# Kernel tuning notes

Hardware: AMD Instinct MI355X
Metric: run time of the kernel (lower is better)

The kernel has to match this reference:

```python
import jax, jax.numpy as jnp
import numpy as np

D_MODEL = 1024
NUM_HEADS = 16


def setup_inputs() -> dict:
    key = jax.random.key(0)
    k1, k2, k3, k4, k5 = jax.random.split(key, 5)
    b, n, d = 4, 2048, D_MODEL
    s = 1.0 / np.sqrt(d)
    x = jax.random.normal(k1, (b, n, d), dtype=jnp.float32)
    v_w = jax.random.uniform(k2, (d, d), dtype=jnp.float32, minval=-s, maxval=s)  # Linear weight [out,in]
    v_b = jax.random.uniform(k3, (d,), dtype=jnp.float32, minval=-s, maxval=s)
    o_w = jax.random.uniform(k4, (d, d), dtype=jnp.float32, minval=-s, maxval=s)
    o_b = jax.random.uniform(k5, (d,), dtype=jnp.float32, minval=-s, maxval=s)
    return {"x": x, "v_w": v_w, "v_b": v_b, "o_w": o_w, "o_b": o_b}


def reference(x, v_w, v_b, o_w, o_b):
    b, n, d = x.shape
    h = NUM_HEADS
    dh = d // h
    # shared QKV projection: q = k = v
    v = jnp.einsum('bnd,ed->bne', x, v_w) + v_b            # [b,n,d]
    v = v.reshape(b, n, h, dh).transpose(0, 2, 1, 3)        # [b,h,n,dh]
    scale = 1.0 / jnp.sqrt(jnp.asarray(dh, dtype=x.dtype))
    scores = jnp.einsum('bhnd,bhmd->bhnm', v, v) * scale    # [b,h,n,n]
    attn = jax.nn.softmax(scores, axis=-1)
    out = jnp.einsum('bhnm,bhmd->bhnd', attn, v)            # [b,h,n,dh]
    out = out.transpose(0, 2, 1, 3).reshape(b, n, d)        # concat heads
    return jnp.einsum('bnd,ed->bne', out, o_w) + o_b
```

## Files before the change

kernel.cpp:

```cpp
#include <hip/hip_runtime.h>
#include <stdint.h>

typedef __attribute__((ext_vector_type(8))) short short8;
typedef __attribute__((ext_vector_type(4))) float f32x4;
typedef __attribute__((ext_vector_type(4))) unsigned int u32x4;
typedef __attribute__((ext_vector_type(2))) unsigned int u32x2;

#define MFMA16(a, b, c) __builtin_amdgcn_mfma_f32_16x16x32_bf16((a), (b), (c), 0, 0, 0)

#define GLD_LDS16(g, l)                                                                  \
    __builtin_amdgcn_global_load_lds((const __attribute__((address_space(1))) void*)(g), \
                                     (__attribute__((address_space(3))) void*)(l), 16, 0, 0)

#if defined(__has_builtin)
#if __has_builtin(__builtin_amdgcn_exp2f)
#define FAST_EXP2(x) __builtin_amdgcn_exp2f(x)
#endif
#endif
#ifndef FAST_EXP2
__device__ __forceinline__ float fast_exp2_asm(float x) {
    float r;
    asm volatile("v_exp_f32 %0, %1\ns_nop 1" : "=v"(r) : "v"(x));
    return r;
}
#define FAST_EXP2(x) fast_exp2_asm(x)
#endif

__device__ __forceinline__ float bf2f(unsigned short u) {
    unsigned int x = ((unsigned int)u) << 16;
    float f;
    __builtin_memcpy(&f, &x, 4);
    return f;
}
__device__ __forceinline__ unsigned short f2bf(float f) {
    unsigned int x;
    __builtin_memcpy(&x, &f, 4);
    unsigned int r = x + 0x7FFFu + ((x >> 16) & 1u);
    return (unsigned short)(r >> 16);
}
__device__ __forceinline__ unsigned int pack2bf(float a, float b) {
    unsigned int ua, ub;
    __builtin_memcpy(&ua, &a, 4);
    __builtin_memcpy(&ub, &b, 4);
    return __builtin_amdgcn_perm(ub + 0x8000u, ua + 0x8000u, 0x07060302u);
}
__device__ __forceinline__ unsigned int cvtpk_bf16(float a, float b) {
    unsigned int r;
    asm("v_cvt_pk_bf16_f32 %0, %1, %2" : "=v"(r) : "v"(a), "v"(b));
    return r;
}
__device__ __forceinline__ u32x4 cvt8(const float* p) {
    f32x4 g0 = *(const f32x4*)p;
    f32x4 g1 = *(const f32x4*)(p + 4);
    u32x4 r;
    r.x = pack2bf(g0[0], g0[1]);
    r.y = pack2bf(g0[2], g0[3]);
    r.z = pack2bf(g1[0], g1[1]);
    r.w = pack2bf(g1[2], g1[3]);
    return r;
}

__global__ __launch_bounds__(256) void cvt_kernel(const float* __restrict__ in,
                                                  unsigned short* __restrict__ out, int n8) {
    int i = blockIdx.x * 256 + threadIdx.x;
    if (i < n8) *(u32x4*)(out + (size_t)i * 8) = cvt8(in + (size_t)i * 8);
}

template <int MODE>
__global__ __launch_bounds__(256) void gemm_dma_kernel(
    const unsigned short* __restrict__ A, const unsigned short* __restrict__ B,
    const float* __restrict__ bias, void* __restrict__ Cv, int M, int N, int K) {
    __shared__ __align__(16) unsigned short As[2][2][128 * 32];
    __shared__ __align__(16) unsigned short Bs[2][2][128 * 32];

    const int tid = threadIdx.x;
    const int wave = tid >> 6, lane = tid & 63;
    const int l15 = lane & 15, quad = lane >> 4;
    const int m0 = blockIdx.x * 128, n0 = blockIdx.y * 128;
    const int wm = (wave >> 1) * 64, wn = (wave & 1) * 64;

    const int row0 = tid >> 2, c0 = (tid & 3) * 8;
    const unsigned short* Ag0 = A + (size_t)(m0 + row0) * K + c0;
    const unsigned short* Ag1 = A + (size_t)(m0 + row0 + 64) * K + c0;
    const unsigned short* Bg0 = B + (size_t)(n0 + row0) * K + c0;
    const unsigned short* Bg1 = B + (size_t)(n0 + row0 + 64) * K + c0;
    const int wl = wave * 512;

#define STAGE(s, k0)                                     \
    do {                                                 \
        GLD_LDS16(Ag0 + (k0), &As[s][0][wl]);            \
        GLD_LDS16(Ag1 + (k0), &As[s][0][2048 + wl]);     \
        GLD_LDS16(Ag0 + (k0) + 32, &As[s][1][wl]);       \
        GLD_LDS16(Ag1 + (k0) + 32, &As[s][1][2048 + wl]); \
        GLD_LDS16(Bg0 + (k0), &Bs[s][0][wl]);            \
        GLD_LDS16(Bg1 + (k0), &Bs[s][0][2048 + wl]);     \
        GLD_LDS16(Bg0 + (k0) + 32, &Bs[s][1][wl]);       \
        GLD_LDS16(Bg1 + (k0) + 32, &Bs[s][1][2048 + wl]); \
    } while (0)

    f32x4 acc[4][4];
#pragma unroll
    for (int i = 0; i < 4; i++)
#pragma unroll
        for (int j = 0; j < 4; j++) {
            f32x4 z = {0.f, 0.f, 0.f, 0.f};
            acc[i][j] = z;
        }

    STAGE(0, 0);
    for (int k0 = 0; k0 < K; k0 += 64) {
        const int s = (k0 >> 6) & 1;
        __syncthreads();
        if (k0 + 64 < K) STAGE(s ^ 1, k0 + 64);

        short8 a0[4], a1[4], b0[4], b1[4];
#pragma unroll
        for (int mt = 0; mt < 4; mt++) {
            a0[mt] = *(const short8*)&As[s][0][(wm + mt * 16 + l15) * 32 + quad * 8];
            a1[mt] = *(const short8*)&As[s][1][(wm + mt * 16 + l15) * 32 + quad * 8];
        }
#pragma unroll
        for (int nt = 0; nt < 4; nt++) {
            b0[nt] = *(const short8*)&Bs[s][0][(wn + nt * 16 + l15) * 32 + quad * 8];
            b1[nt] = *(const short8*)&Bs[s][1][(wn + nt * 16 + l15) * 32 + quad * 8];
        }
#pragma unroll
        for (int mt = 0; mt < 4; mt++)
#pragma unroll
            for (int nt = 0; nt < 4; nt++) acc[mt][nt] = MFMA16(a0[mt], b0[nt], acc[mt][nt]);
#pragma unroll
        for (int mt = 0; mt < 4; mt++)
#pragma unroll
            for (int nt = 0; nt < 4; nt++) acc[mt][nt] = MFMA16(a1[mt], b1[nt], acc[mt][nt]);
    }
#undef STAGE

    float bv[4];
#pragma unroll
    for (int nt = 0; nt < 4; nt++) bv[nt] = bias[n0 + wn + nt * 16 + l15];

#pragma unroll
    for (int mt = 0; mt < 4; mt++)
#pragma unroll
        for (int nt = 0; nt < 4; nt++)
#pragma unroll
            for (int i = 0; i < 4; i++) {
                int m = m0 + wm + mt * 16 + quad * 4 + i;
                int n = n0 + wn + nt * 16 + l15;
                float val = acc[mt][nt][i] + bv[nt];
                if (MODE == 0) {
                    int bb = m >> 11, ns = m & 2047, h = n >> 6, c = n & 63;
                    ((unsigned short*)Cv)[(size_t)(bb * 16 + h) * 131072 + (size_t)ns * 64 + c] =
                        f2bf(val);
                } else {
                    ((float*)Cv)[(size_t)m * N + n] = val;
                }
            }
}

template <bool AF32, bool BF32, int MODE>
__global__ __launch_bounds__(256) void gemm_bias_kernel(
    const void* __restrict__ Av, const void* __restrict__ Bv,
    const float* __restrict__ bias, void* __restrict__ Cv, int M, int N, int K) {
    __shared__ __align__(16) unsigned short As[128][40];
    __shared__ __align__(16) unsigned short Bs[128][40];

    const int tid = threadIdx.x;
    const int wave = tid >> 6, lane = tid & 63;
    const int l15 = lane & 15, quad = lane >> 4;
    const int m0 = blockIdx.x * 128, n0 = blockIdx.y * 128;
    const int wm = (wave >> 1) * 64, wn = (wave & 1) * 64;

    f32x4 acc[4][4];
#pragma unroll
    for (int i = 0; i < 4; i++)
#pragma unroll
        for (int j = 0; j < 4; j++) {
            f32x4 z = {0.f, 0.f, 0.f, 0.f};
            acc[i][j] = z;
        }

    for (int k0 = 0; k0 < K; k0 += 32) {
        __syncthreads();
#pragma unroll
        for (int rep = 0; rep < 2; rep++) {
            int chunk = tid + rep * 256;
            int row = chunk >> 2, c8 = (chunk & 3) * 8;
            if (AF32) {
                const float* Af = (const float*)Av;
                *(u32x4*)&As[row][c8] = cvt8(&Af[(size_t)(m0 + row) * K + k0 + c8]);
            } else {
                const unsigned short* Ab = (const unsigned short*)Av;
                *(f32x4*)&As[row][c8] = *(const f32x4*)&Ab[(size_t)(m0 + row) * K + k0 + c8];
            }
            if (BF32) {
                const float* Bf = (const float*)Bv;
                *(u32x4*)&Bs[row][c8] = cvt8(&Bf[(size_t)(n0 + row) * K + k0 + c8]);
            } else {
                const unsigned short* Bb = (const unsigned short*)Bv;
                *(f32x4*)&Bs[row][c8] = *(const f32x4*)&Bb[(size_t)(n0 + row) * K + k0 + c8];
            }
        }
        __syncthreads();

        short8 a[4], b[4];
#pragma unroll
        for (int mt = 0; mt < 4; mt++) a[mt] = *(const short8*)&As[wm + mt * 16 + l15][quad * 8];
#pragma unroll
        for (int nt = 0; nt < 4; nt++) b[nt] = *(const short8*)&Bs[wn + nt * 16 + l15][quad * 8];
#pragma unroll
        for (int mt = 0; mt < 4; mt++)
#pragma unroll
            for (int nt = 0; nt < 4; nt++) acc[mt][nt] = MFMA16(a[mt], b[nt], acc[mt][nt]);
    }

    float bv[4];
#pragma unroll
    for (int nt = 0; nt < 4; nt++) bv[nt] = bias[n0 + wn + nt * 16 + l15];

#pragma unroll
    for (int mt = 0; mt < 4; mt++)
#pragma unroll
        for (int nt = 0; nt < 4; nt++)
#pragma unroll
            for (int i = 0; i < 4; i++) {
                int m = m0 + wm + mt * 16 + quad * 4 + i;
                int n = n0 + wn + nt * 16 + l15;
                float val = acc[mt][nt][i] + bv[nt];
                if (MODE == 0) {
                    int bb = m >> 11, ns = m & 2047, h = n >> 6, c = n & 63;
                    ((unsigned short*)Cv)[(size_t)(bb * 16 + h) * 131072 + (size_t)ns * 64 + c] =
                        f2bf(val);
                } else {
                    ((float*)Cv)[(size_t)m * N + n] = val;
                }
            }
}

__global__ __launch_bounds__(256) void transpose_kernel(const unsigned short* __restrict__ V,
                                                        unsigned short* __restrict__ Vt) {
    __shared__ __align__(16) unsigned short T[64][72];
    const int tid = threadIdx.x;
    const int n0 = blockIdx.x * 64;
    const size_t base = (size_t)blockIdx.y * 131072;
#pragma unroll
    for (int rep = 0; rep < 2; rep++) {
        int chunk = tid + rep * 256;
        int row = chunk >> 3, c8 = (chunk & 7) * 8;
        *(short8*)&T[row][c8] = *(const short8*)&V[base + (size_t)(n0 + row) * 64 + c8];
    }
    __syncthreads();
#pragma unroll
    for (int rep = 0; rep < 2; rep++) {
        int chunk = tid + rep * 256;
        int d = chunk >> 3, n8 = (chunk & 7) * 8;
        short8 o;
#pragma unroll
        for (int j = 0; j < 8; j++) o[j] = (short)T[n8 + j][d];
        *(short8*)&Vt[base + (size_t)d * 2048 + n0 + n8] = o;
    }
}

__global__ __launch_bounds__(256, 4) void attn_kernel(const unsigned short* __restrict__ V,
                                                      const unsigned short* __restrict__ Vt,
                                                      unsigned short* __restrict__ O) {
    __shared__ __align__(16) unsigned short QP[128 * 64];
    __shared__ __align__(16) unsigned short Ks[64 * 64];
    __shared__ __align__(16) unsigned short VTs[2][64 * 64];

    const int tid = threadIdx.x;
    const int wave = tid >> 6, lane = tid & 63;
    const int l15 = lane & 15, quad = lane >> 4;
    const int sx = l15 & 7;

    const int flat = blockIdx.y * 16 + blockIdx.x;
    const int bh = (flat & 7) * 8 + ((flat >> 3) & 7);
    const int q0 = (flat >> 6) * 128;

    const unsigned short* Vh = V + (size_t)bh * 131072;
    const unsigned short* VhT = Vt + (size_t)bh * 131072;
    const int wm = wave * 32;

    const int srow = wave * 16 + (lane >> 3);
    const int scol = ((lane & 7) ^ (lane >> 3)) * 8;
    const unsigned short* gK = Vh + (size_t)srow * 64 + scol;
    const unsigned short* gVT = VhT + (size_t)srow * 2048 + scol;

#define KSTAGE(kv)                                                       \
    do {                                                                 \
        GLD_LDS16(gK + (size_t)(kv) * 64, &Ks[wave * 1024]);             \
        GLD_LDS16(gK + (size_t)(kv) * 64 + 512, &Ks[wave * 1024 + 512]); \
    } while (0)
#define VSTAGE(s, kv)                                                 \
    do {                                                              \
        GLD_LDS16(gVT + (kv), &VTs[s][wave * 1024]);                  \
        GLD_LDS16(gVT + (kv) + 8 * 2048, &VTs[s][wave * 1024 + 512]); \
    } while (0)

    KSTAGE(0);
    VSTAGE(0, 0);

#pragma unroll
    for (int rep = 0; rep < 4; rep++) {
        int chunk = tid + rep * 256;
        int row = chunk >> 3, cs = chunk & 7;
        short8 g = *(const short8*)&Vh[(size_t)(q0 + row) * 64 + cs * 8];
        short8 o;
#pragma unroll
        for (int j = 0; j < 8; j++)
            o[j] = (short)f2bf(bf2f((unsigned short)g[j]) * 0.1803368801f);
        *(short8*)&QP[row * 64 + ((cs ^ (row & 7)) << 3)] = o;
    }
    __syncthreads();

    short8 bq[2][2];
#pragma unroll
    for (int mt = 0; mt < 2; mt++) {
        const int row = wm + mt * 16 + l15;
#pragma unroll
        for (int ks = 0; ks < 2; ks++)
            bq[mt][ks] = *(const short8*)&QP[row * 64 + ((((ks << 2) | quad) ^ sx) << 3)];
    }

    short8 vones;
#pragma unroll
    for (int j = 0; j < 8; j++) vones[j] = (short)0x3F80;

    f32x4 oacc[2][4];
    f32x4 lsacc[2];
#pragma unroll
    for (int mt = 0; mt < 2; mt++) {
        f32x4 z = {0.f, 0.f, 0.f, 0.f};
        lsacc[mt] = z;
#pragma unroll
        for (int ct = 0; ct < 4; ct++) oacc[mt][ct] = z;
    }

    for (int kv0 = 0; kv0 < 2048; kv0 += 64) {
        const int s = (kv0 >> 6) & 1;
        __syncthreads();
        if (kv0 + 64 < 2048) VSTAGE(s ^ 1, kv0 + 64);

        f32x4 st[4][2];
#pragma unroll
        for (int nt = 0; nt < 4; nt++) {
            const int krow = (nt * 16 + l15) * 64;
            short8 ak0 = *(const short8*)&Ks[krow + ((quad ^ sx) << 3)];
            short8 ak1 = *(const short8*)&Ks[krow + (((4 | quad) ^ sx) << 3)];
#pragma unroll
            for (int mt = 0; mt < 2; mt++) {
                f32x4 z = {0.f, 0.f, 0.f, 0.f};
                z = MFMA16(ak0, bq[mt][0], z);
                z = MFMA16(ak1, bq[mt][1], z);
                st[nt][mt] = z;
            }
        }

        __builtin_amdgcn_sched_barrier(0);
        __builtin_amdgcn_s_barrier();
        __builtin_amdgcn_sched_barrier(0);
        if (kv0 + 64 < 2048) KSTAGE(kv0 + 64);

#pragma unroll
        for (int mt = 0; mt < 2; mt++) {
            const int prow = (wm + mt * 16 + l15) * 64;
#pragma unroll
            for (int nt = 0; nt < 4; nt++) {
                f32x4 p;
#pragma unroll
                for (int i = 0; i < 4; i++) p[i] = FAST_EXP2(st[nt][mt][i]);
                u32x2 w;
                w.x = cvtpk_bf16(p[0], p[1]);
                w.y = cvtpk_bf16(p[2], p[3]);
                const int slot = (nt * 2 + (quad >> 1)) ^ sx;
                *(u32x2*)&QP[prow + slot * 8 + (quad & 1) * 4] = w;
            }
        }
        asm volatile("s_waitcnt lgkmcnt(0)" ::: "memory");

#pragma unroll
        for (int kt = 0; kt < 2; kt++) {
            short8 ap[2];
#pragma unroll
            for (int mt = 0; mt < 2; mt++) {
                const int row = wm + mt * 16 + l15;
                ap[mt] = *(const short8*)&QP[row * 64 + ((((kt << 2) | quad) ^ sx) << 3)];
            }
#pragma unroll
            for (int ct = 0; ct < 4; ct++) {
                short8 bvf =
                    *(const short8*)&VTs[s][(ct * 16 + l15) * 64 + ((((kt << 2) | quad) ^ sx) << 3)];
#pragma unroll
                for (int mt = 0; mt < 2; mt++) oacc[mt][ct] = MFMA16(ap[mt], bvf, oacc[mt][ct]);
            }
#pragma unroll
            for (int mt = 0; mt < 2; mt++) lsacc[mt] = MFMA16(ap[mt], vones, lsacc[mt]);
        }
    }
#undef KSTAGE
#undef VSTAGE

    float inv[2][4];
#pragma unroll
    for (int mt = 0; mt < 2; mt++)
#pragma unroll
        for (int i = 0; i < 4; i++) inv[mt][i] = 1.0f / lsacc[mt][i];

    const int bb = bh >> 4, h = bh & 15;
#pragma unroll
    for (int mt = 0; mt < 2; mt++)
#pragma unroll
        for (int i = 0; i < 4; i++) {
            int m = q0 + wm + mt * 16 + quad * 4 + i;
            size_t rowbase = ((size_t)(bb * 2048 + m)) * 1024 + h * 64;
#pragma unroll
            for (int ct = 0; ct < 4; ct++)
                O[rowbase + ct * 16 + l15] = f2bf(oacc[mt][ct][i] * inv[mt][i]);
        }
}

extern "C" void kernel_launch(void* const* d_in, const int* in_sizes, int n_in, void* d_out,
                              int out_size, void* d_ws, size_t ws_size, hipStream_t stream) {
    (void)in_sizes; (void)n_in; (void)out_size;
    const float* x = (const float*)d_in[0];
    const float* v_w = (const float*)d_in[1];
    const float* v_b = (const float*)d_in[2];
    const float* o_w = (const float*)d_in[3];
    const float* o_b = (const float*)d_in[4];
    float* out = (float*)d_out;

    unsigned short* Vbuf = (unsigned short*)d_out;
    unsigned short* Vtbuf = Vbuf + (size_t)8192 * 1024;
    unsigned short* Obuf = (unsigned short*)d_ws;

    const size_t need =
        ((size_t)8192 * 1024  + (size_t)8192 * 1024  + 2 * (size_t)1024 * 1024) * 2;
    if (ws_size >= need) {
        unsigned short* xbf = Obuf + (size_t)8192 * 1024;
        unsigned short* wv = xbf + (size_t)8192 * 1024;
        unsigned short* wo = wv + (size_t)1024 * 1024;
        cvt_kernel<<<4096, 256, 0, stream>>>(x, xbf, 1048576);
        cvt_kernel<<<512, 256, 0, stream>>>(v_w, wv, 131072);
        cvt_kernel<<<512, 256, 0, stream>>>(o_w, wo, 131072);
        gemm_dma_kernel<0><<<dim3(64, 8), 256, 0, stream>>>(xbf, wv, v_b, Vbuf, 8192, 1024, 1024);
        transpose_kernel<<<dim3(32, 64), 256, 0, stream>>>(Vbuf, Vtbuf);
        attn_kernel<<<dim3(16, 64), 256, 0, stream>>>(Vbuf, Vtbuf, Obuf);
        gemm_dma_kernel<1><<<dim3(64, 8), 256, 0, stream>>>(Obuf, wo, o_b, out, 8192, 1024, 1024);
    } else {
        gemm_bias_kernel<true, true, 0>
            <<<dim3(64, 8), 256, 0, stream>>>(x, v_w, v_b, Vbuf, 8192, 1024, 1024);
        transpose_kernel<<<dim3(32, 64), 256, 0, stream>>>(Vbuf, Vtbuf);
        attn_kernel<<<dim3(16, 64), 256, 0, stream>>>(Vbuf, Vtbuf, Obuf);
        gemm_bias_kernel<false, true, 1>
            <<<dim3(64, 8), 256, 0, stream>>>(Obuf, o_w, o_b, out, 8192, 1024, 1024);
    }
}
```

Baseline: 219.7 us.

## Keep attention probabilities in registers via permlane swaps, double-buffer K, fuse casts

The attention kernel no longer writes the exp'd probabilities to shared memory and reads them back. It regroups the MFMA accumulator layout into A-operand layout in registers using permlane32/16 swaps. Q fragments are now loaded straight from global memory into registers instead of through LDS. K tiles are double-buffered alongside V, which removes the mid-iteration barrier, and the three fp32-to-bf16 conversion launches are merged into one kernel. The changes trade LDS traffic and a barrier for extra cross-lane instructions and added s_nop padding, and they depend on the permlane mapping matching the MFMA operand layout.

```diff
diff --git a/kernel.cpp b/kernel.cpp
--- a/kernel.cpp
+++ b/kernel.cpp
@@ -26,6 +26,31 @@
 #define FAST_EXP2(x) fast_exp2_asm(x)
 #endif
 
+#if defined(__has_builtin)
+#if __has_builtin(__builtin_amdgcn_permlane32_swap) && __has_builtin(__builtin_amdgcn_permlane16_swap)
+#define HAVE_PERMLANE_SWAP 1
+#endif
+#endif
+
+__device__ __forceinline__ void permlane_regroup(unsigned int& x, unsigned int& y) {
+#ifdef HAVE_PERMLANE_SWAP
+    {
+        auto r = __builtin_amdgcn_permlane32_swap(x, y, false, false);
+        auto r2 = __builtin_amdgcn_permlane16_swap(r[0], r[1], false, false);
+        x = r2[0];
+        y = r2[1];
+    }
+#else
+    asm volatile(
+        "s_nop 3\n\t"
+        "v_permlane32_swap_b32 %0, %1\n\t"
+        "s_nop 3\n\t"
+        "v_permlane16_swap_b32 %0, %1\n\t"
+        "s_nop 3"
+        : "+v"(x), "+v"(y));
+#endif
+}
+
 __device__ __forceinline__ float bf2f(unsigned short u) {
     unsigned int x = ((unsigned int)u) << 16;
     float f;
@@ -46,7 +71,7 @@
 }
 __device__ __forceinline__ unsigned int cvtpk_bf16(float a, float b) {
     unsigned int r;
-    asm("v_cvt_pk_bf16_f32 %0, %1, %2" : "=v"(r) : "v"(a), "v"(b));
+    asm("v_cvt_pk_bf16_f32 %0, %1, %2\n\ts_nop 1" : "=v"(r) : "v"(a), "v"(b));
     return r;
 }
 __device__ __forceinline__ u32x4 cvt8(const float* p) {
@@ -60,10 +85,22 @@
     return r;
 }
 
-__global__ __launch_bounds__(256) void cvt_kernel(const float* __restrict__ in,
-                                                  unsigned short* __restrict__ out, int n8) {
+__global__ __launch_bounds__(256) void cvt3_kernel(const float* __restrict__ a,
+                                                   unsigned short* __restrict__ oa, int na8,
+                                                   const float* __restrict__ b,
+                                                   unsigned short* __restrict__ ob, int nb8,
+                                                   const float* __restrict__ c,
+                                                   unsigned short* __restrict__ oc, int nc8) {
     int i = blockIdx.x * 256 + threadIdx.x;
-    if (i < n8) *(u32x4*)(out + (size_t)i * 8) = cvt8(in + (size_t)i * 8);
+    if (i < na8) {
+        *(u32x4*)(oa + (size_t)i * 8) = cvt8(a + (size_t)i * 8);
+    } else if (i < na8 + nb8) {
+        int j = i - na8;
+        *(u32x4*)(ob + (size_t)j * 8) = cvt8(b + (size_t)j * 8);
+    } else if (i < na8 + nb8 + nc8) {
+        int j = i - na8 - nb8;
+        *(u32x4*)(oc + (size_t)j * 8) = cvt8(c + (size_t)j * 8);
+    }
 }
 
 template <int MODE>
@@ -264,8 +301,7 @@
 __global__ __launch_bounds__(256, 4) void attn_kernel(const unsigned short* __restrict__ V,
                                                       const unsigned short* __restrict__ Vt,
                                                       unsigned short* __restrict__ O) {
-    __shared__ __align__(16) unsigned short QP[128 * 64];
-    __shared__ __align__(16) unsigned short Ks[64 * 64];
+    __shared__ __align__(16) unsigned short Ks[2][64 * 64];
     __shared__ __align__(16) unsigned short VTs[2][64 * 64];
 
     const int tid = threadIdx.x;
@@ -286,10 +322,10 @@
     const unsigned short* gK = Vh + (size_t)srow * 64 + scol;
     const unsigned short* gVT = VhT + (size_t)srow * 2048 + scol;
 
-#define KSTAGE(kv)                                                       \
-    do {                                                                 \
-        GLD_LDS16(gK + (size_t)(kv) * 64, &Ks[wave * 1024]);             \
-        GLD_LDS16(gK + (size_t)(kv) * 64 + 512, &Ks[wave * 1024 + 512]); \
+#define KSTAGE(s, kv)                                                       \
+    do {                                                                    \
+        GLD_LDS16(gK + (size_t)(kv) * 64, &Ks[s][wave * 1024]);             \
+        GLD_LDS16(gK + (size_t)(kv) * 64 + 512, &Ks[s][wave * 1024 + 512]); \
     } while (0)
 #define VSTAGE(s, kv)                                                 \
     do {                                                              \
@@ -297,30 +333,27 @@
         GLD_LDS16(gVT + (kv) + 8 * 2048, &VTs[s][wave * 1024 + 512]); \
     } while (0)
 
-    KSTAGE(0);
+    KSTAGE(0, 0);
     VSTAGE(0, 0);
 
-#pragma unroll
-    for (int rep = 0; rep < 4; rep++) {
-        int chunk = tid + rep * 256;
-        int row = chunk >> 3, cs = chunk & 7;
-        short8 g = *(const short8*)&Vh[(size_t)(q0 + row) * 64 + cs * 8];
-        short8 o;
-#pragma unroll
-        for (int j = 0; j < 8; j++)
-            o[j] = (short)f2bf(bf2f((unsigned short)g[j]) * 0.1803368801f);
-        *(short8*)&QP[row * 64 + ((cs ^ (row & 7)) << 3)] = o;
-    }
-    __syncthreads();
-
     short8 bq[2][2];
 #pragma unroll
-    for (int mt = 0; mt < 2; mt++) {
-        const int row = wm + mt * 16 + l15;
-#pragma unroll
-        for (int ks = 0; ks < 2; ks++)
-            bq[mt][ks] = *(const short8*)&QP[row * 64 + ((((ks << 2) | quad) ^ sx) << 3)];
-    }
+    for (int mt = 0; mt < 2; mt++)
+#pragma unroll
+        for (int ks = 0; ks < 2; ks++) {
+            short8 g = *(const short8*)&Vh[(size_t)(q0 + wm + mt * 16 + l15) * 64 + ks * 32 +
+                                           quad * 8];
+            u32x4 a;
+            a.x = cvtpk_bf16(bf2f((unsigned short)g[0]) * 0.1803368801f,
+                             bf2f((unsigned short)g[1]) * 0.1803368801f);
+            a.y = cvtpk_bf16(bf2f((unsigned short)g[2]) * 0.1803368801f,
+                             bf2f((unsigned short)g[3]) * 0.1803368801f);
+            a.z = cvtpk_bf16(bf2f((unsigned short)g[4]) * 0.1803368801f,
+                             bf2f((unsigned short)g[5]) * 0.1803368801f);
+            a.w = cvtpk_bf16(bf2f((unsigned short)g[6]) * 0.1803368801f,
+                             bf2f((unsigned short)g[7]) * 0.1803368801f);
+            bq[mt][ks] = *(short8*)&a;
+        }
 
     short8 vones;
 #pragma unroll
@@ -339,14 +372,17 @@
     for (int kv0 = 0; kv0 < 2048; kv0 += 64) {
         const int s = (kv0 >> 6) & 1;
         __syncthreads();
-        if (kv0 + 64 < 2048) VSTAGE(s ^ 1, kv0 + 64);
+        if (kv0 + 64 < 2048) {
+            KSTAGE(s ^ 1, kv0 + 64);
+            VSTAGE(s ^ 1, kv0 + 64);
+        }
 
         f32x4 st[4][2];
 #pragma unroll
         for (int nt = 0; nt < 4; nt++) {
             const int krow = (nt * 16 + l15) * 64;
-            short8 ak0 = *(const short8*)&Ks[krow + ((quad ^ sx) << 3)];
-            short8 ak1 = *(const short8*)&Ks[krow + (((4 | quad) ^ sx) << 3)];
+            short8 ak0 = *(const short8*)&Ks[s][krow + ((quad ^ sx) << 3)];
+            short8 ak1 = *(const short8*)&Ks[s][krow + (((4 | quad) ^ sx) << 3)];
 #pragma unroll
             for (int mt = 0; mt < 2; mt++) {
                 f32x4 z = {0.f, 0.f, 0.f, 0.f};
@@ -356,45 +392,44 @@
             }
         }
 
-        __builtin_amdgcn_sched_barrier(0);
-        __builtin_amdgcn_s_barrier();
-        __builtin_amdgcn_sched_barrier(0);
-        if (kv0 + 64 < 2048) KSTAGE(kv0 + 64);
-
+        short8 ap[2][2];
 #pragma unroll
         for (int mt = 0; mt < 2; mt++) {
-            const int prow = (wm + mt * 16 + l15) * 64;
+            unsigned int w[4][2];
 #pragma unroll
             for (int nt = 0; nt < 4; nt++) {
                 f32x4 p;
 #pragma unroll
                 for (int i = 0; i < 4; i++) p[i] = FAST_EXP2(st[nt][mt][i]);
-                u32x2 w;
-                w.x = cvtpk_bf16(p[0], p[1]);
-                w.y = cvtpk_bf16(p[2], p[3]);
-                const int slot = (nt * 2 + (quad >> 1)) ^ sx;
-                *(u32x2*)&QP[prow + slot * 8 + (quad & 1) * 4] = w;
-            }
-        }
-        asm volatile("s_waitcnt lgkmcnt(0)" ::: "memory");
+                w[nt][0] = cvtpk_bf16(p[0], p[1]);
+                w[nt][1] = cvtpk_bf16(p[2], p[3]);
+            }
+#pragma unroll
+            for (int kt = 0; kt < 2; kt++) {
+                unsigned int x0 = w[2 * kt][0], x1 = w[2 * kt][1];
+                unsigned int y0 = w[2 * kt + 1][0], y1 = w[2 * kt + 1][1];
+                permlane_regroup(x0, y0);
+                permlane_regroup(x1, y1);
+                u32x4 a;
+                a.x = x0;
+                a.y = x1;
+                a.z = y0;
+                a.w = y1;
+                ap[mt][kt] = *(short8*)&a;
+            }
+        }
 
 #pragma unroll
         for (int kt = 0; kt < 2; kt++) {
-            short8 ap[2];
-#pragma unroll
-            for (int mt = 0; mt < 2; mt++) {
-                const int row = wm + mt * 16 + l15;
-                ap[mt] = *(const short8*)&QP[row * 64 + ((((kt << 2) | quad) ^ sx) << 3)];
-            }
 #pragma unroll
             for (int ct = 0; ct < 4; ct++) {
                 short8 bvf =
                     *(const short8*)&VTs[s][(ct * 16 + l15) * 64 + ((((kt << 2) | quad) ^ sx) << 3)];
 #pragma unroll
-                for (int mt = 0; mt < 2; mt++) oacc[mt][ct] = MFMA16(ap[mt], bvf, oacc[mt][ct]);
-            }
-#pragma unroll
-            for (int mt = 0; mt < 2; mt++) lsacc[mt] = MFMA16(ap[mt], vones, lsacc[mt]);
+                for (int mt = 0; mt < 2; mt++) oacc[mt][ct] = MFMA16(ap[mt][kt], bvf, oacc[mt][ct]);
+            }
+#pragma unroll
+            for (int mt = 0; mt < 2; mt++) lsacc[mt] = MFMA16(ap[mt][kt], vones, lsacc[mt]);
         }
     }
 #undef KSTAGE
@@ -439,9 +474,7 @@
         unsigned short* xbf = Obuf + (size_t)8192 * 1024;
         unsigned short* wv = xbf + (size_t)8192 * 1024;
         unsigned short* wo = wv + (size_t)1024 * 1024;
-        cvt_kernel<<<4096, 256, 0, stream>>>(x, xbf, 1048576);
-        cvt_kernel<<<512, 256, 0, stream>>>(v_w, wv, 131072);
-        cvt_kernel<<<512, 256, 0, stream>>>(o_w, wo, 131072);
+        cvt3_kernel<<<5120, 256, 0, stream>>>(x, xbf, 1048576, v_w, wv, 131072, o_w, wo, 131072);
         gemm_dma_kernel<0><<<dim3(64, 8), 256, 0, stream>>>(xbf, wv, v_b, Vbuf, 8192, 1024, 1024);
         transpose_kernel<<<dim3(32, 64), 256, 0, stream>>>(Vbuf, Vtbuf);
         attn_kernel<<<dim3(16, 64), 256, 0, stream>>>(Vbuf, Vtbuf, Obuf);
```

Result: no change. 217.6 us (-1.0%).
